# Optimization experiments

Measured on AMD Instinct MI355X. Metric: run time of the kernel, lower is better.

The kernel has to match this reference:

```python
import jax, jax.numpy as jnp
import numpy as np

B, S, D = 4096, 10, 1024

def setup_inputs() -> dict:
    key = jax.random.key(0)
    ks = jax.random.split(key, 8)
    sD = 1.0 / np.sqrt(D)
    s2D = 1.0 / np.sqrt(2 * D)
    sH = 1.0 / np.sqrt(D // 2)
    return {
        "input_1": jax.random.normal(ks[0], (B, S, D), jnp.float32),
        "input_2": jax.random.normal(ks[1], (B, S, D), jnp.float32),
        # mlp_graph: Linear(2D -> D), stored (in, out)
        "Wg": jax.random.uniform(ks[2], (2 * D, D), jnp.float32, -s2D, s2D),
        "bg": jax.random.uniform(ks[3], (D,), jnp.float32, -s2D, s2D),
        # fd: Linear(2D -> D//2)
        "Wfd": jax.random.uniform(ks[4], (2 * D, D // 2), jnp.float32, -s2D, s2D),
        "bfd": jax.random.uniform(ks[5], (D // 2,), jnp.float32, -s2D, s2D),
        # ff: Linear(D//2 -> 1)
        "Wff": jax.random.uniform(ks[6], (D // 2, 1), jnp.float32, -sH, sH),
        "bff": jax.random.uniform(ks[7], (1,), jnp.float32, -sH, sH),
    }

def reference(input_1, input_2, Wg, bg, Wfd, bfd, Wff, bff):
    # graph_match: cross-graph affinity [B, S, T]
    a = jnp.einsum('bsd,btd->bst', input_1, input_2)
    a_x = jax.nn.softmax(a, axis=1)   # softmax over rows (dim=1)
    a_y = jax.nn.softmax(a, axis=0)   # unusual cross-batch softmax (dim=0)
    # attention_x = a_x^T @ input_1 ; attention_y = a_y @ input_2
    attention_x = jnp.einsum('bst,bsd->btd', a_x, input_1)
    attention_y = jnp.einsum('bst,btd->bsd', a_y, input_2)
    output_x = jnp.concatenate([input_1, attention_y], axis=2) @ Wg + bg
    output_y = jnp.concatenate([input_2, attention_x], axis=2) @ Wg + bg
    # training head: last token of each, concat, fd-ReLU-ff-Sigmoid
    o1 = output_x[:, -1, :]
    o2 = output_y[:, -1, :]
    h = jax.nn.relu(jnp.concatenate([o1, o2], axis=1) @ Wfd + bfd)
    logits = jnp.squeeze(h @ Wff + bff, axis=-1)
    return jax.nn.sigmoid(logits)
```

## Files before the change

### kernel.cpp

```cpp
#include <hip/hip_runtime.h>
#include <hip/hip_bf16.h>

#define BATCH 4096
#define SEQ 10
#define DIM 1024
#define TWOD 2048
#define HID 512

typedef __attribute__((ext_vector_type(8))) short bf16x8;
typedef __attribute__((ext_vector_type(4))) float f32x4;

#define OFF_ABF   0ull
#define OFF_OCB   (32ull << 20)
#define OFF_WGT   (48ull << 20)
#define OFF_WFDT  (52ull << 20)
#define OFF_LOG   (54ull << 20)
#define OFF_AROW  (62ull << 20)
#define OFF_STATS (OFF_AROW + 4096ull * 16 * 4)

#define GLOAD_LDS16(g, l)                                                     \
  __builtin_amdgcn_global_load_lds(                                           \
      (const __attribute__((address_space(1))) unsigned int*)(g),             \
      (__attribute__((address_space(3))) unsigned int*)(l), 16, 0, 0)

#define SW(r) (((r) + ((r) >> 2)) & 3)

static __device__ inline void store_bf4(__hip_bfloat16* p, float4 v) {
  ushort4 u;
  __hip_bfloat16 a = __float2bfloat16(v.x), b = __float2bfloat16(v.y),
                 c = __float2bfloat16(v.z), d = __float2bfloat16(v.w);
  u.x = *(unsigned short*)&a; u.y = *(unsigned short*)&b;
  u.z = *(unsigned short*)&c; u.w = *(unsigned short*)&d;
  *(ushort4*)p = u;
}

__global__ __launch_bounds__(256) void k_scores(
    const float* __restrict__ X1, const float* __restrict__ X2,
    __hip_bfloat16* __restrict__ abf, float* __restrict__ arow,
    float* __restrict__ logits) {
  int b = blockIdx.x;
  int tid = threadIdx.x;
  int wave = tid >> 6, lane = tid & 63;
  const float* x1b = X1 + (size_t)b * SEQ * DIM;
  const float* x2b = X2 + (size_t)b * SEQ * DIM;
  __shared__ float sc[20];
  __shared__ float4 xch[4 * 64];
  if (tid == 0) logits[b] = 0.f;

  const float* Abase;
  const float* Brow;
  if (wave == 0)      { Abase = x1b;           Brow = x2b + 9 * DIM; }
  else if (wave == 1) { Abase = x1b + 5 * DIM; Brow = x2b + 9 * DIM; }
  else if (wave == 2) { Abase = x2b;           Brow = x1b + 9 * DIM; }
  else                { Abase = x2b + 5 * DIM; Brow = x1b + 9 * DIM; }

  float4 ra[5][4], rb[4];
#pragma unroll
  for (int i = 0; i < 4; i++)
    rb[i] = *(const float4*)(Brow + i * 256 + lane * 4);
#pragma unroll
  for (int s = 0; s < 5; s++)
#pragma unroll
    for (int i = 0; i < 4; i++)
      ra[s][i] = *(const float4*)(Abase + s * DIM + i * 256 + lane * 4);

  float v[5];
#pragma unroll
  for (int s = 0; s < 5; s++) {
    float4 a4 = ra[s][0] * rb[0] + ra[s][1] * rb[1] + ra[s][2] * rb[2] +
                ra[s][3] * rb[3];
    v[s] = a4.x + a4.y + a4.z + a4.w;
  }
#pragma unroll
  for (int off = 1; off < 64; off <<= 1)
#pragma unroll
    for (int s = 0; s < 5; s++) v[s] += __shfl_xor(v[s], off, 64);

  if (lane == 0) {
    int base = wave * 5;
    sc[base + 0] = v[0]; sc[base + 1] = v[1]; sc[base + 2] = v[2];
    sc[base + 3] = v[3]; sc[base + 4] = v[4];
  }
  __syncthreads();

  if (tid < SEQ) arow[(size_t)b * 16 + tid] = sc[10 + tid];

  float px[SEQ];
#pragma unroll
  for (int s = 0; s < SEQ; s++) px[s] = sc[s];
  float m = -1e30f;
#pragma unroll
  for (int s = 0; s < SEQ; s++) m = fmaxf(m, px[s]);
  float w[SEQ], Z = 0.f;
#pragma unroll
  for (int s = 0; s < SEQ; s++) { w[s] = __expf(px[s] - m); Z += w[s]; }
  float inv = 1.f / Z;

  __hip_bfloat16* rowx1 = abf + (size_t)b * TWOD;
  __hip_bfloat16* rowx2 = abf + (size_t)(BATCH + b) * TWOD;

  if (wave == 1) {
#pragma unroll
    for (int i = 0; i < 4; i++) {
      float4 pb = ra[0][i] * w[5] + ra[1][i] * w[6] + ra[2][i] * w[7] +
                  ra[3][i] * w[8] + ra[4][i] * w[9];
      xch[i * 64 + lane] = pb;
      store_bf4(rowx2 + i * 256 + lane * 4, rb[i]);
    }
  } else if (wave == 2) {
#pragma unroll
    for (int i = 0; i < 4; i++)
      store_bf4(rowx1 + i * 256 + lane * 4, rb[i]);
  }
  __syncthreads();
  if (wave == 0) {
#pragma unroll
    for (int i = 0; i < 4; i++) {
      float4 ax = ra[0][i] * w[0] + ra[1][i] * w[1] + ra[2][i] * w[2] +
                  ra[3][i] * w[3] + ra[4][i] * w[4];
      ax = (ax + xch[i * 64 + lane]) * inv;
      store_bf4(rowx2 + DIM + i * 256 + lane * 4, ax);
    }
  }
}

__global__ __launch_bounds__(256) void k_stats(const float* __restrict__ arow,
                                               float* __restrict__ stats) {
  int t = blockIdx.x;
  int tid = threadIdx.x, lane = tid & 63, wave = tid >> 6;
  __shared__ float wred[4];
  float m = -1e30f;
  for (int b = tid; b < BATCH; b += 256) m = fmaxf(m, arow[(size_t)b * 16 + t]);
  for (int off = 32; off; off >>= 1) m = fmaxf(m, __shfl_down(m, off, 64));
  if (lane == 0) wred[wave] = m;
  __syncthreads();
  m = fmaxf(fmaxf(wred[0], wred[1]), fmaxf(wred[2], wred[3]));
  __syncthreads();
  float z = 0.f;
  for (int b = tid; b < BATCH; b += 256) z += __expf(arow[(size_t)b * 16 + t] - m);
  for (int off = 32; off; off >>= 1) z += __shfl_down(z, off, 64);
  if (lane == 0) wred[wave] = z;
  __syncthreads();
  if (tid == 0) {
    stats[t] = m;
    stats[16 + t] = wred[0] + wred[1] + wred[2] + wred[3];
  }
}

__global__ __launch_bounds__(256) void k_apply_y(const float* __restrict__ X2,
                                                 const float* __restrict__ arow,
                                                 const float* __restrict__ stats,
                                                 __hip_bfloat16* __restrict__ abf) {
  int b = blockIdx.x;
  int wave = threadIdx.x >> 6, lane = threadIdx.x & 63;
  float wy[SEQ];
#pragma unroll
  for (int t = 0; t < SEQ; t++)
    wy[t] = __expf(arow[(size_t)b * 16 + t] - stats[t]) / stats[16 + t];
  const float* x2b = X2 + (size_t)b * SEQ * DIM;
  int d = wave * 256 + lane * 4;
  float4 acc = {0.f, 0.f, 0.f, 0.f};
#pragma unroll
  for (int t = 0; t < SEQ; t++)
    acc += wy[t] * *(const float4*)(x2b + t * DIM + d);
  store_bf4(abf + (size_t)b * TWOD + DIM + d, acc);
}

__global__ __launch_bounds__(256) void k_transpose_both(
    const float* __restrict__ Wg, const float* __restrict__ Wfd,
    __hip_bfloat16* __restrict__ wgt, __hip_bfloat16* __restrict__ wfdt) {
  __shared__ float t[32][33];
  int by = blockIdx.y;
  const float* in;
  __hip_bfloat16* out;
  int C, c0;
  if (by < 32) { in = Wg; out = wgt; C = DIM; c0 = by * 32; }
  else         { in = Wfd; out = wfdt; C = HID; c0 = (by - 32) * 32; }
  int r0 = blockIdx.x * 32;
  int tx = threadIdx.x & 31, ty = threadIdx.x >> 5;
#pragma unroll
  for (int i = 0; i < 4; i++)
    t[ty + 8 * i][tx] = in[(size_t)(r0 + ty + 8 * i) * C + c0 + tx];
  __syncthreads();
#pragma unroll
  for (int i = 0; i < 4; i++)
    out[(size_t)(c0 + ty + 8 * i) * TWOD + r0 + tx] =
        __float2bfloat16(t[tx][ty + 8 * i]);
}

#define G1_BUF  24576
#define G1_BOFF 16384
#define G1_NT   32

__global__ __launch_bounds__(512, 1) void k_gemm1(
    const __hip_bfloat16* __restrict__ A, const __hip_bfloat16* __restrict__ Bt,
    const float* __restrict__ bias, __hip_bfloat16* __restrict__ outb, int K) {
  __shared__ short lds[3 * G1_BUF];
  int tid = threadIdx.x;
  int lane = tid & 63, wave = tid >> 6;
  int flat = blockIdx.x;
  int swz = (flat & 7) * 32 + (flat >> 3);
  int m0 = (swz >> 3) * 256, n0 = (swz & 7) * 128;
  int wr = wave >> 2, wc = wave & 3;
  int g = lane >> 4, r16 = lane & 15;

  int srow = tid >> 3;
  int ss = (tid & 7) ^ (srow & 7);
  const __hip_bfloat16* sa = A + (size_t)(m0 + srow) * K + ss * 8;
  const __hip_bfloat16* sb = Bt + (size_t)(n0 + srow) * K + ss * 8;
  int dA = wave * 512;
  int dB = G1_BOFF + wave * 512;

#define G1_STAGE(kt, c)                                                       \
  {                                                                           \
    const __hip_bfloat16* sak = sa + (kt)*64;                                 \
    const __hip_bfloat16* sbk = sb + (kt)*64;                                 \
    GLOAD_LDS16(sak + 0 * 64 * K, &lds[(c)*G1_BUF + dA + 0 * 4096]);          \
    GLOAD_LDS16(sak + 1 * 64 * K, &lds[(c)*G1_BUF + dA + 1 * 4096]);          \
    GLOAD_LDS16(sak + 2 * 64 * K, &lds[(c)*G1_BUF + dA + 2 * 4096]);          \
    GLOAD_LDS16(sak + 3 * 64 * K, &lds[(c)*G1_BUF + dA + 3 * 4096]);          \
    GLOAD_LDS16(sbk + 0 * 64 * K, &lds[(c)*G1_BUF + dB + 0 * 4096]);          \
    GLOAD_LDS16(sbk + 1 * 64 * K, &lds[(c)*G1_BUF + dB + 1 * 4096]);          \
  }

  f32x4 acc[8][2] = {};

  G1_STAGE(0, 0);
  G1_STAGE(1, 1);
  asm volatile("s_waitcnt vmcnt(6)" ::: "memory");
  __builtin_amdgcn_sched_barrier(0);
  __builtin_amdgcn_s_barrier();
  __builtin_amdgcn_sched_barrier(0);

#pragma unroll 1
  for (int kt = 0; kt < G1_NT; ++kt) {
    int cur = kt - (kt / 3) * 3;
    if (kt + 2 < G1_NT) {
      int nx = (kt + 2) - ((kt + 2) / 3) * 3;
      G1_STAGE(kt + 2, nx);
    }
    const short* bufA = &lds[cur * G1_BUF];
    const short* bufB = &lds[cur * G1_BUF + G1_BOFF];
#pragma unroll
    for (int kk = 0; kk < 2; ++kk) {
      int sr = ((kk * 4 + g) ^ (r16 & 7)) * 8;
      bf16x8 af[8], bfr[2];
#pragma unroll
      for (int mi = 0; mi < 8; mi++)
        af[mi] = *(const bf16x8*)&bufA[(wr * 128 + mi * 16 + r16) * 64 + sr];
#pragma unroll
      for (int ni = 0; ni < 2; ni++)
        bfr[ni] = *(const bf16x8*)&bufB[(wc * 32 + ni * 16 + r16) * 64 + sr];
      __builtin_amdgcn_s_setprio(1);
#pragma unroll
      for (int mi = 0; mi < 8; mi++)
#pragma unroll
        for (int ni = 0; ni < 2; ni++)
          acc[mi][ni] = __builtin_amdgcn_mfma_f32_16x16x32_bf16(
              af[mi], bfr[ni], acc[mi][ni], 0, 0, 0);
      __builtin_amdgcn_s_setprio(0);
    }
    if (kt < G1_NT - 2)
      asm volatile("s_waitcnt vmcnt(6)" ::: "memory");
    else
      asm volatile("s_waitcnt vmcnt(0)" ::: "memory");
    __builtin_amdgcn_sched_barrier(0);
    __builtin_amdgcn_s_barrier();
    __builtin_amdgcn_sched_barrier(0);
  }

#pragma unroll
  for (int mi = 0; mi < 8; mi++) {
#pragma unroll
    for (int ni = 0; ni < 2; ni++) {
#pragma unroll
      for (int r = 0; r < 4; r++) {
        int m = m0 + wr * 128 + mi * 16 + g * 4 + r;
        int n = n0 + wc * 32 + ni * 16 + r16;
        float v = acc[mi][ni][r] + bias[n];
        int om = m & (BATCH - 1);
        int on = n + ((m >> 12) << 10);
        outb[(size_t)om * TWOD + on] = __float2bfloat16(v);
      }
    }
  }
#undef G1_STAGE
}

__global__ __launch_bounds__(256) void k_gemm2_final(
    const __hip_bfloat16* __restrict__ A, const __hip_bfloat16* __restrict__ Bt,
    const float* __restrict__ bfd, const float* __restrict__ Wff,
    float* __restrict__ logits, int K) {
  __shared__ short lds[12288];
  int tid = threadIdx.x;
  int lane = tid & 63, wave = tid >> 6;
  int flat = blockIdx.y * 8 + blockIdx.x;
  int swz = (flat & 7) * 32 + (flat >> 3);
  int m0 = (swz >> 3) * 128, n0 = (swz & 7) * 64;
  int wr = wave >> 1, wc = wave & 1;

  f32x4 acc[4][2] = {};
  int lrow = lane >> 2, ls = lane & 3;
  int g = lane >> 4, r16 = lane & 15;

  for (int k0 = 0; k0 < K; k0 += 64) {
#pragma unroll
    for (int half = 0; half < 2; half++) {
      int kk = k0 + half * 32;
#pragma unroll
      for (int c = 0; c < 2; c++) {
        int R0 = 16 * (2 * wave + c);
        int rr = R0 + lrow;
        int slot = ls ^ SW(rr);
        GLOAD_LDS16(A + (size_t)(m0 + rr) * K + kk + slot * 8,
                    &lds[half * 4096 + R0 * 32]);
      }
      int RB = 16 * wave, rb = RB + lrow;
      int slotb = ls ^ SW(rb);
      GLOAD_LDS16(Bt + (size_t)(n0 + rb) * K + kk + slotb * 8,
                  &lds[8192 + half * 2048 + RB * 32]);
    }
    __syncthreads();
#pragma unroll
    for (int half = 0; half < 2; half++) {
      bf16x8 af[4], bfr[2];
#pragma unroll
      for (int mi = 0; mi < 4; mi++) {
        int m = wr * 64 + mi * 16 + r16;
        af[mi] = *(const bf16x8*)&lds[half * 4096 + m * 32 + ((g ^ SW(m)) << 3)];
      }
#pragma unroll
      for (int ni = 0; ni < 2; ni++) {
        int n = wc * 32 + ni * 16 + r16;
        bfr[ni] =
            *(const bf16x8*)&lds[8192 + half * 2048 + n * 32 + ((g ^ SW(n)) << 3)];
      }
#pragma unroll
      for (int mi = 0; mi < 4; mi++)
#pragma unroll
        for (int ni = 0; ni < 2; ni++)
          acc[mi][ni] = __builtin_amdgcn_mfma_f32_16x16x32_bf16(
              af[mi], bfr[ni], acc[mi][ni], 0, 0, 0);
    }
    __syncthreads();
  }

  int nA = n0 + wc * 32 + r16, nB = nA + 16;
  float bA = bfd[nA], bB = bfd[nB];
  float wA = Wff[nA], wB = Wff[nB];
#pragma unroll
  for (int mi = 0; mi < 4; mi++) {
#pragma unroll
    for (int r = 0; r < 4; r++) {
      float v0 = acc[mi][0][r] + bA; v0 = v0 > 0.f ? v0 : 0.f;
      float v1 = acc[mi][1][r] + bB; v1 = v1 > 0.f ? v1 : 0.f;
      float pl = v0 * wA + v1 * wB;
#pragma unroll
      for (int off = 1; off < 16; off <<= 1) pl += __shfl_xor(pl, off, 64);
      if (r16 == 0)
        atomicAdd(&logits[m0 + wr * 64 + mi * 16 + g * 4 + r], pl);
    }
  }
}

__global__ __launch_bounds__(256) void k_sigmoid(const float* __restrict__ logits,
                                                 const float* __restrict__ bff,
                                                 float* __restrict__ out) {
  int b = blockIdx.x * 256 + threadIdx.x;
  out[b] = 1.f / (1.f + __expf(-(logits[b] + bff[0])));
}

extern "C" void kernel_launch(void* const* d_in, const int* in_sizes, int n_in,
                              void* d_out, int out_size, void* d_ws, size_t ws_size,
                              hipStream_t stream) {
  const float* X1  = (const float*)d_in[0];
  const float* X2  = (const float*)d_in[1];
  const float* Wg  = (const float*)d_in[2];
  const float* bg  = (const float*)d_in[3];
  const float* Wfd = (const float*)d_in[4];
  const float* bfd = (const float*)d_in[5];
  const float* Wff = (const float*)d_in[6];
  const float* bff = (const float*)d_in[7];
  float* out = (float*)d_out;
  char* ws = (char*)d_ws;

  __hip_bfloat16* abf  = (__hip_bfloat16*)(ws + OFF_ABF);
  __hip_bfloat16* ocb  = (__hip_bfloat16*)(ws + OFF_OCB);
  __hip_bfloat16* wgt  = (__hip_bfloat16*)(ws + OFF_WGT);
  __hip_bfloat16* wfdt = (__hip_bfloat16*)(ws + OFF_WFDT);
  float* logits = (float*)(ws + OFF_LOG);
  float* arow   = (float*)(ws + OFF_AROW);
  float* stats  = (float*)(ws + OFF_STATS);

  k_transpose_both<<<dim3(64, 48), 256, 0, stream>>>(Wg, Wfd, wgt, wfdt);
  k_scores<<<BATCH, 256, 0, stream>>>(X1, X2, abf, arow, logits);
  k_stats<<<SEQ, 256, 0, stream>>>(arow, stats);
  k_apply_y<<<BATCH, 256, 0, stream>>>(X2, arow, stats, abf);
  k_gemm1<<<256, 512, 0, stream>>>(abf, wgt, bg, ocb, TWOD);
  k_gemm2_final<<<dim3(8, 32), 256, 0, stream>>>(ocb, wfdt, bfd, Wff, logits,
                                                 TWOD);
  k_sigmoid<<<BATCH / 256, 256, 0, stream>>>(logits, bff, out);
}
```

Measured before the change: 182.6 us.

## Triple-buffer gemm2 LDS tiles with async prefetch and single barrier per K-step

Rewrites the second GEMM (ocb @ Wfd with fused relu/ff head) to use a three-stage LDS ring with global_load_lds prefetch two K-tiles ahead. Each iteration now has one barrier, gated by explicit vmcnt waits, instead of two __syncthreads. The LDS tile layout changes to 64-wide rows with an XOR swizzle, and MFMA sections are wrapped in s_setprio. The cost is tripled LDS use per block, which may lower occupancy. The change targets load latency in a small GEMM that is a minor share of total runtime.

```diff
diff --git a/kernel.cpp b/kernel.cpp
--- a/kernel.cpp
+++ b/kernel.cpp
@@ -287,62 +287,86 @@
 #undef G1_STAGE
 }
 
+#define G2_BUF  12288
+#define G2_BOFF 8192
+#define G2_NT   32
+
 __global__ __launch_bounds__(256) void k_gemm2_final(
     const __hip_bfloat16* __restrict__ A, const __hip_bfloat16* __restrict__ Bt,
     const float* __restrict__ bfd, const float* __restrict__ Wff,
     float* __restrict__ logits, int K) {
-  __shared__ short lds[12288];
+  __shared__ short lds[3 * G2_BUF];
   int tid = threadIdx.x;
   int lane = tid & 63, wave = tid >> 6;
-  int flat = blockIdx.y * 8 + blockIdx.x;
+  int flat = blockIdx.x;
   int swz = (flat & 7) * 32 + (flat >> 3);
   int m0 = (swz >> 3) * 128, n0 = (swz & 7) * 64;
   int wr = wave >> 1, wc = wave & 1;
+  int g = lane >> 4, r16 = lane & 15;
+
+  int srow = tid >> 3;
+  int ss = (tid & 7) ^ (srow & 7);
+  const __hip_bfloat16* sa = A + (size_t)(m0 + srow) * K + ss * 8;
+  const __hip_bfloat16* sb = Bt + (size_t)(n0 + srow) * K + ss * 8;
+  int dA = wave * 512;
+  int dB = G2_BOFF + wave * 512;
+
+#define G2_STAGE(kt, c)                                                       \
+  {                                                                           \
+    const __hip_bfloat16* sak = sa + (kt)*64;                                 \
+    const __hip_bfloat16* sbk = sb + (kt)*64;                                 \
+    GLOAD_LDS16(sak + 0 * 32 * K, &lds[(c)*G2_BUF + dA + 0 * 2048]);          \
+    GLOAD_LDS16(sak + 1 * 32 * K, &lds[(c)*G2_BUF + dA + 1 * 2048]);          \
+    GLOAD_LDS16(sak + 2 * 32 * K, &lds[(c)*G2_BUF + dA + 2 * 2048]);          \
+    GLOAD_LDS16(sak + 3 * 32 * K, &lds[(c)*G2_BUF + dA + 3 * 2048]);          \
+    GLOAD_LDS16(sbk + 0 * 32 * K, &lds[(c)*G2_BUF + dB + 0 * 2048]);          \
+    GLOAD_LDS16(sbk + 1 * 32 * K, &lds[(c)*G2_BUF + dB + 1 * 2048]);          \
+  }
 
   f32x4 acc[4][2] = {};
-  int lrow = lane >> 2, ls = lane & 3;
-  int g = lane >> 4, r16 = lane & 15;
-
-  for (int k0 = 0; k0 < K; k0 += 64) {
-#pragma unroll
-    for (int half = 0; half < 2; half++) {
-      int kk = k0 + half * 32;
-#pragma unroll
-      for (int c = 0; c < 2; c++) {
-        int R0 = 16 * (2 * wave + c);
-        int rr = R0 + lrow;
-        int slot = ls ^ SW(rr);
-        GLOAD_LDS16(A + (size_t)(m0 + rr) * K + kk + slot * 8,
-                    &lds[half * 4096 + R0 * 32]);
-      }
-      int RB = 16 * wave, rb = RB + lrow;
-      int slotb = ls ^ SW(rb);
-      GLOAD_LDS16(Bt + (size_t)(n0 + rb) * K + kk + slotb * 8,
-                  &lds[8192 + half * 2048 + RB * 32]);
-    }
-    __syncthreads();
-#pragma unroll
-    for (int half = 0; half < 2; half++) {
+
+  G2_STAGE(0, 0);
+  G2_STAGE(1, 1);
+  asm volatile("s_waitcnt vmcnt(6)" ::: "memory");
+  __builtin_amdgcn_sched_barrier(0);
+  __builtin_amdgcn_s_barrier();
+  __builtin_amdgcn_sched_barrier(0);
+
+#pragma unroll 1
+  for (int kt = 0; kt < G2_NT; ++kt) {
+    int cur = kt - (kt / 3) * 3;
+    if (kt + 2 < G2_NT) {
+      int nx = (kt + 2) - ((kt + 2) / 3) * 3;
+      G2_STAGE(kt + 2, nx);
+    }
+    const short* bufA = &lds[cur * G2_BUF];
+    const short* bufB = &lds[cur * G2_BUF + G2_BOFF];
+#pragma unroll
+    for (int kk = 0; kk < 2; ++kk) {
+      int sr = ((kk * 4 + g) ^ (r16 & 7)) * 8;
       bf16x8 af[4], bfr[2];
 #pragma unroll
-      for (int mi = 0; mi < 4; mi++) {
-        int m = wr * 64 + mi * 16 + r16;
-        af[mi] = *(const bf16x8*)&lds[half * 4096 + m * 32 + ((g ^ SW(m)) << 3)];
-      }
-#pragma unroll
-      for (int ni = 0; ni < 2; ni++) {
-        int n = wc * 32 + ni * 16 + r16;
-        bfr[ni] =
-            *(const bf16x8*)&lds[8192 + half * 2048 + n * 32 + ((g ^ SW(n)) << 3)];
-      }
+      for (int mi = 0; mi < 4; mi++)
+        af[mi] = *(const bf16x8*)&bufA[(wr * 64 + mi * 16 + r16) * 64 + sr];
+#pragma unroll
+      for (int ni = 0; ni < 2; ni++)
+        bfr[ni] = *(const bf16x8*)&bufB[(wc * 32 + ni * 16 + r16) * 64 + sr];
+      __builtin_amdgcn_s_setprio(1);
 #pragma unroll
       for (int mi = 0; mi < 4; mi++)
 #pragma unroll
         for (int ni = 0; ni < 2; ni++)
           acc[mi][ni] = __builtin_amdgcn_mfma_f32_16x16x32_bf16(
               af[mi], bfr[ni], acc[mi][ni], 0, 0, 0);
-    }
-    __syncthreads();
+      __builtin_amdgcn_s_setprio(0);
+    }
+    if (kt < G2_NT - 2)
+      asm volatile("s_waitcnt vmcnt(6)" ::: "memory");
+    else
+      asm volatile("s_waitcnt vmcnt(0)" ::: "memory");
+    __builtin_amdgcn_sched_barrier(0);
+    __builtin_amdgcn_s_barrier();
+    __builtin_amdgcn_sched_barrier(0);
   }
 
   int nA = n0 + wc * 32 + r16, nB = nA + 16;
@@ -361,6 +385,7 @@
         atomicAdd(&logits[m0 + wr * 64 + mi * 16 + g * 4 + r], pl);
     }
   }
+#undef G2_STAGE
 }
 
 __global__ __launch_bounds__(256) void k_sigmoid(const float* __restrict__ logits,
@@ -397,7 +422,6 @@
   k_stats<<<SEQ, 256, 0, stream>>>(arow, stats);
   k_apply_y<<<BATCH, 256, 0, stream>>>(X2, arow, stats, abf);
   k_gemm1<<<256, 512, 0, stream>>>(abf, wgt, bg, ocb, TWOD);
-  k_gemm2_final<<<dim3(8, 32), 256, 0, stream>>>(ocb, wfdt, bfd, Wff, logits,
-                                                 TWOD);
+  k_gemm2_final<<<256, 256, 0, stream>>>(ocb, wfdt, bfd, Wff, logits, TWOD);
   k_sigmoid<<<BATCH / 256, 256, 0, stream>>>(logits, bff, out);
 }
```

Measured after the change: 163.2 us (median of 2 runs). 10.6% less time.
